# Optimization experiments

Hardware: AMD Instinct MI355X
Metric: run time of the kernel (lower is better)

## Reference

```python
import jax, jax.numpy as jnp
import numpy as np
from jax import lax

H = 256        # HIDDEN_DIM
H2 = 2 * H     # BiLSTM output dim
L = 100        # MAX_SENTENCE_LENGHT
B = 16
WE = 100       # word embed size
PE = 50        # pos embed size
VOC = 46       # POS_VOCAB_SIZE + 1
IN0 = WE + PE  # lstm layer-0 input dim


def setup_inputs():
    key = jax.random.key(0)
    ks = jax.random.split(key, 20)
    s = 0.05
    inp = {}
    inp["word_embeds"] = jax.random.normal(ks[0], (B, L, WE), jnp.float32)
    inp["pos_idx"] = jax.random.randint(ks[1], (B, L), 0, VOC)
    inp["sen_lens"] = jax.random.randint(ks[2], (B,), 1, L + 1)
    inp["pos_emb"] = jax.random.normal(ks[3], (VOC, PE), jnp.float32) * s
    # LSTM layer 0 (input dim 150), directions stacked on axis 0 (fwd, rev)
    inp["w_ih0"] = jax.random.normal(ks[4], (2, 4 * H, IN0), jnp.float32) * s
    inp["w_hh0"] = jax.random.normal(ks[5], (2, 4 * H, H), jnp.float32) * s
    inp["b_ih0"] = jax.random.normal(ks[6], (2, 4 * H), jnp.float32) * s
    inp["b_hh0"] = jax.random.normal(ks[7], (2, 4 * H), jnp.float32) * s
    # LSTM layers 1-3 (input dim 512): [layer, dir, ...]
    inp["w_ih"] = jax.random.normal(ks[8], (3, 2, 4 * H, H2), jnp.float32) * s
    inp["w_hh"] = jax.random.normal(ks[9], (3, 2, 4 * H, H), jnp.float32) * s
    inp["b_ih"] = jax.random.normal(ks[10], (3, 2, 4 * H), jnp.float32) * s
    inp["b_hh"] = jax.random.normal(ks[11], (3, 2, 4 * H), jnp.float32) * s
    # PosTagFC: Linear(1024,512), Linear(512,128), Linear(128,1)
    inp["W1"] = jax.random.normal(ks[12], (H2, 2 * H2), jnp.float32) * s
    inp["b1"] = jax.random.normal(ks[13], (H2,), jnp.float32) * s
    inp["W2"] = jax.random.normal(ks[14], (H // 2, H2), jnp.float32) * s
    inp["b2"] = jax.random.normal(ks[15], (H // 2,), jnp.float32) * s
    inp["W3"] = jax.random.normal(ks[16], (1, H // 2), jnp.float32) * s
    inp["b3"] = jax.random.normal(ks[17], (1,), jnp.float32) * s
    return inp


def _lstm_dir(x, wi, wh, bi, bh, reverse):
    # x: [B, L, F]; PyTorch gate order i, f, g, o
    gx = jnp.einsum('blf,gf->blg', x, wi) + bi + bh  # [B, L, 4H]
    xs = jnp.swapaxes(gx, 0, 1)                      # [L, B, 4H]
    if reverse:
        xs = xs[::-1]
    h0 = jnp.zeros((x.shape[0], H), x.dtype)
    def step(carry, g):
        h, c = carry
        g = g + h @ wh.T
        i, f, gg, o = jnp.split(g, 4, axis=-1)
        c = jax.nn.sigmoid(f) * c + jax.nn.sigmoid(i) * jnp.tanh(gg)
        h = jax.nn.sigmoid(o) * jnp.tanh(c)
        return (h, c), h
    _, hs = lax.scan(step, (h0, h0), xs)
    hs = jnp.swapaxes(hs, 0, 1)                      # [B, L, H]
    if reverse:
        hs = hs[:, ::-1]
    return hs


def _forward(word_embeds, pos_idx, sen_lens, pos_emb,
             w_ih0, w_hh0, b_ih0, b_hh0, w_ih, w_hh, b_ih, b_hh,
             W1, b1, W2, b2, W3, b3):
    x = jnp.concatenate([word_embeds, pos_emb[pos_idx]], axis=2)  # [B, L, 150]
    # 4-layer bidirectional LSTM (eval mode: inter-layer dropout off)
    fwd = _lstm_dir(x, w_ih0[0], w_hh0[0], b_ih0[0], b_hh0[0], False)
    bwd = _lstm_dir(x, w_ih0[1], w_hh0[1], b_ih0[1], b_hh0[1], True)
    x = jnp.concatenate([fwd, bwd], axis=-1)
    for l in range(3):
        fwd = _lstm_dir(x, w_ih[l, 0], w_hh[l, 0], b_ih[l, 0], b_hh[l, 0], False)
        bwd = _lstm_dir(x, w_ih[l, 1], w_hh[l, 1], b_ih[l, 1], b_hh[l, 1], True)
        x = jnp.concatenate([fwd, bwd], axis=-1)  # [B, L, 512]
    lstm_out = x
    # pairwise scoring: split W1 so we never materialize the 1024-dim concat
    rooted = jnp.concatenate([jnp.zeros((B, 1, H2), x.dtype), lstm_out], axis=1)  # [B, L+1, 512]
    W1a, W1b = W1[:, :H2], W1[:, H2:]
    h_first = lstm_out @ W1a.T          # [B, L, 512]
    h_root = rooted @ W1b.T             # [B, L+1, 512]
    h1 = jax.nn.relu(h_first[:, :, None, :] + h_root[:, None, :, :] + b1)  # [B, L, L+1, 512]
    h2 = jax.nn.relu(h1 @ W2.T + b2)    # [B, L, L+1, 128]
    sc = (h2 @ W3.T + b3)[..., 0]       # [B, L, L+1]
    # fill_diagonal_ on the [N,1] fc output zeroes only element 0 -> (0,0)
    sc = sc.at[:, 0, 0].set(0.0)
    row_ok = jnp.arange(L)[None, :] < sen_lens[:, None]        # [B, L]
    col_ok = jnp.arange(L + 1)[None, :] <= sen_lens[:, None]   # [B, L+1]
    sc = jnp.where(row_ok[:, :, None] & col_ok[:, None, :], sc, 0.0)
    return jnp.pad(sc, ((0, 0), (0, 1), (0, 0)))  # [B, 101, 101]


def reference(word_embeds, pos_idx, sen_lens, pos_emb,
              w_ih0, w_hh0, b_ih0, b_hh0, w_ih, w_hh, b_ih, b_hh,
              W1, b1, W2, b2, W3, b3):
    return _forward(word_embeds, pos_idx, sen_lens, pos_emb,
                    w_ih0, w_hh0, b_ih0, b_hh0, w_ih, w_hh, b_ih, b_hh,
                    W1, b1, W2, b2, W3, b3)
```

## Files before the change

kernel.cpp:

```cpp
#include <hip/hip_runtime.h>
#include <stdint.h>

#define NB 16
#define NL 100
#define NOUT (16*101*101)

typedef _Float16 f16x8 __attribute__((ext_vector_type(8)));
typedef float f32x4 __attribute__((ext_vector_type(4)));

__device__ __forceinline__ float sigm(float x) {
    x = fminf(fmaxf(x, -30.f), 30.f);
    return 1.f / (1.f + __expf(-x));
}
__device__ __forceinline__ float tanh_(float x) {
    x = fminf(fmaxf(x, -15.f), 15.f);
    float t = __expf(2.f * x);
    return (t - 1.f) / (t + 1.f);
}
__device__ __forceinline__ uint32_t pack2h(_Float16 a, _Float16 b) {
    return (uint32_t)__builtin_bit_cast(uint16_t, a) |
           ((uint32_t)__builtin_bit_cast(uint16_t, b) << 16);
}
#define MFMA16(A, B, C) __builtin_amdgcn_mfma_f32_16x16x32_f16( \
    __builtin_bit_cast(f16x8, A), (B), (C), 0, 0, 0)


__global__ __launch_bounds__(256) void pack_whh_mfma(const float* __restrict__ w_hh0,
                                                     const float* __restrict__ w_hh,
                                                     uint32_t* __restrict__ wpk) {
    int idx = blockIdx.x * 256 + threadIdx.x;
    if (idx >= 262144) return;
    int l6 = idx & 63;
    int kc = (idx >> 6) & 7;
    int mt = (idx >> 9) & 63;
    int ld = idx >> 15;
    int layer = ld >> 1, d = ld & 1;
    int row = mt * 16 + (l6 & 15);
    int k0 = kc * 32 + (l6 >> 4) * 8;
    const float* src = (layer == 0)
        ? &w_hh0[((size_t)d * 1024 + row) * 256]
        : &w_hh[(((size_t)(layer - 1) * 2 + d) * 1024 + row) * 256];
    uint4 o;
    o.x = pack2h((_Float16)src[k0 + 0], (_Float16)src[k0 + 1]);
    o.y = pack2h((_Float16)src[k0 + 2], (_Float16)src[k0 + 3]);
    o.z = pack2h((_Float16)src[k0 + 4], (_Float16)src[k0 + 5]);
    o.w = pack2h((_Float16)src[k0 + 6], (_Float16)src[k0 + 7]);
    *(uint4*)&wpk[(size_t)idx * 4] = o;
}

__global__ __launch_bounds__(256) void pack_wih(const float* __restrict__ w_ih0,
                                                const float* __restrict__ w_ih,
                                                uint32_t* __restrict__ wihpk) {
    int idx = blockIdx.x * 256 + threadIdx.x;
    if (idx >= 524288) return;
    int l6 = idx & 63;
    int kc = (idx >> 6) & 15;
    int mt = (idx >> 10) & 63;
    int dl = idx >> 16;
    int row = mt * 16 + (l6 & 15);
    int k0 = kc * 32 + (l6 >> 4) * 8;
    float v[8];
#pragma unroll
    for (int j = 0; j < 8; ++j) {
        int k = k0 + j;
        if (dl < 2) v[j] = (k < 150) ? w_ih0[((size_t)dl * 1024 + row) * 150 + k] : 0.f;
        else        v[j] = w_ih[((size_t)(dl - 2) * 1024 + row) * 512 + k];
    }
    uint4 o;
    o.x = pack2h((_Float16)v[0], (_Float16)v[1]);
    o.y = pack2h((_Float16)v[2], (_Float16)v[3]);
    o.z = pack2h((_Float16)v[4], (_Float16)v[5]);
    o.w = pack2h((_Float16)v[6], (_Float16)v[7]);
    *(uint4*)&wihpk[(size_t)idx * 4] = o;
}

__global__ __launch_bounds__(256) void pack_w1(const float* __restrict__ W1,
                                               uint32_t* __restrict__ w1pk) {
    int idx = blockIdx.x * 256 + threadIdx.x;
    if (idx >= 65536) return;
    int l6 = idx & 63;
    int kc = (idx >> 6) & 15;
    int mt = (idx >> 10) & 31;
    int half = idx >> 15;
    int row = mt * 16 + (l6 & 15);
    int k0 = kc * 32 + (l6 >> 4) * 8;
    const float* src = &W1[(size_t)row * 1024 + half * 512 + k0];
    uint4 o;
    o.x = pack2h((_Float16)src[0], (_Float16)src[1]);
    o.y = pack2h((_Float16)src[2], (_Float16)src[3]);
    o.z = pack2h((_Float16)src[4], (_Float16)src[5]);
    o.w = pack2h((_Float16)src[6], (_Float16)src[7]);
    *(uint4*)&w1pk[(size_t)idx * 4] = o;
}

__global__ __launch_bounds__(256) void pack_w2_mfma(const float* __restrict__ W2,
                                                    uint32_t* __restrict__ w2pk) {
    int idx = blockIdx.x * 256 + threadIdx.x;
    if (idx >= 16384) return;
    int l6 = idx & 63;
    int nt = (idx >> 6) & 7;
    int sp = (idx >> 9) & 1;
    int kc = idx >> 10;
    int ch = nt * 16 + (l6 & 15);
    int k0 = kc * 32 + (l6 >> 4) * 8;
    uint32_t dw[4];
#pragma unroll
    for (int dwi = 0; dwi < 4; ++dwi) {
        float x0 = W2[(size_t)ch * 512 + k0 + dwi * 2 + 0];
        float x1 = W2[(size_t)ch * 512 + k0 + dwi * 2 + 1];
        _Float16 h0 = (_Float16)x0, h1 = (_Float16)x1;
        _Float16 v0 = sp ? (_Float16)(x0 - (float)h0) : h0;
        _Float16 v1 = sp ? (_Float16)(x1 - (float)h1) : h1;
        dw[dwi] = pack2h(v0, v1);
    }
    *(uint4*)&w2pk[(size_t)idx * 4] = make_uint4(dw[0], dw[1], dw[2], dw[3]);
}

__global__ __launch_bounds__(256) void pack_bias(const float* __restrict__ b_ih0,
                                                 const float* __restrict__ b_hh0,
                                                 const float* __restrict__ b_ih,
                                                 const float* __restrict__ b_hh,
                                                 float* __restrict__ biasp) {
    int idx = blockIdx.x * 256 + threadIdx.x;
    if (idx >= 8 * 1024) return;
    int g = idx & 1023;
    int ld = idx >> 10;
    int l = ld >> 1, d = ld & 1;
    float v;
    if (l == 0) v = b_ih0[d * 1024 + g] + b_hh0[d * 1024 + g];
    else {
        size_t o = ((size_t)(l - 1) * 2 + d) * 1024 + g;
        v = b_ih[o] + b_hh[o];
    }
    biasp[idx] = v;
}

__global__ __launch_bounds__(256) void concat_x0v2(const float* __restrict__ we,
                                                   const int* __restrict__ pos_idx,
                                                   const float* __restrict__ pos_emb,
                                                   _Float16* __restrict__ xhi,
                                                   _Float16* __restrict__ xlo) {
    int idx = blockIdx.x * 256 + threadIdx.x;
    if (idx >= 1600 * 160) return;
    int mp = idx / 160, k = idx % 160;
    int tt = mp >> 4, b = mp & 15;
    float v;
    if (k < 100) v = we[((size_t)b * 100 + tt) * 100 + k];
    else if (k < 150) v = pos_emb[(size_t)pos_idx[b * 100 + tt] * 50 + (k - 100)];
    else v = 0.f;
    _Float16 hi = (_Float16)v;
    xhi[idx] = hi;
    xlo[idx] = (_Float16)(v - (float)hi);
}

__global__ __launch_bounds__(256) void zero_out(float* __restrict__ out) {
    int idx = blockIdx.x * 256 + threadIdx.x;
    if (idx < NOUT) out[idx] = 0.f;
}

__global__ __launch_bounds__(256) void gemm_gx(const _Float16* __restrict__ xhi,
                                               const _Float16* __restrict__ xlo,
                                               const uint32_t* __restrict__ wpk_base,
                                               const float* __restrict__ bias_base,
                                               float* __restrict__ gxf_base,
                                               int KC, int ldx) {
    const int d = blockIdx.z;
    const uint32_t* wpk = wpk_base + (size_t)d * 262144;
    const float* bias = bias_base + d * 1024;
    float* gxf_d = gxf_base + (size_t)d * 1638400;

    const int t = threadIdx.x;
    const int wv = t >> 6, l = t & 63;
    const int cgrp = l >> 4;
    const int m0t = blockIdx.x * 4;
    const int n0 = blockIdx.y * 64;
    const int tk0 = n0 + wv * 16 + (l & 15);

    f32x4 acc[4];
#pragma unroll
    for (int mt = 0; mt < 4; ++mt) acc[mt] = (f32x4){0.f, 0.f, 0.f, 0.f};

    for (int kc = 0; kc < KC; ++kc) {
        const int koff = kc * 32 + cgrp * 8;
        f16x8 bh = *(const f16x8*)&xhi[(size_t)tk0 * ldx + koff];
        f16x8 bl = *(const f16x8*)&xlo[(size_t)tk0 * ldx + koff];
#pragma unroll
        for (int mt = 0; mt < 4; ++mt) {
            uint4 a = *(const uint4*)&wpk[(((size_t)(m0t + mt) * 16 + kc) * 64 + l) * 4];
            acc[mt] = MFMA16(a, bh, acc[mt]);
            acc[mt] = MFMA16(a, bl, acc[mt]);
        }
    }
    const int b = l & 15;
    const int tt = tk0 >> 4;
#pragma unroll
    for (int mt = 0; mt < 4; ++mt) {
        int mtg = m0t + mt;
        f32x4 bv;
#pragma unroll
        for (int r = 0; r < 4; ++r) bv[r] = bias[mtg * 16 + cgrp * 4 + r];
        size_t off = ((size_t)b * 100 + tt) * 1024 + mtg * 16 + cgrp * 4;
        *(f32x4*)&gxf_d[off] = acc[mt] + bv;
    }
}

__global__ __launch_bounds__(256) void gemm_w1(const _Float16* __restrict__ xhi,
                                               const _Float16* __restrict__ xlo,
                                               const uint32_t* __restrict__ wpk_base,
                                               float* __restrict__ outp) {
    const int half = blockIdx.z;
    const uint32_t* wpk = wpk_base + (size_t)half * 131072;
    const int coff = half * 512;

    const int t = threadIdx.x;
    const int wv = t >> 6, l = t & 63;
    const int cgrp = l >> 4;
    const int m0t = blockIdx.x * 4;
    const int n0 = blockIdx.y * 64;
    const int tk0 = n0 + wv * 16 + (l & 15);

    f32x4 acc[4];
#pragma unroll
    for (int mt = 0; mt < 4; ++mt) acc[mt] = (f32x4){0.f, 0.f, 0.f, 0.f};

    for (int kc = 0; kc < 16; ++kc) {
        const int koff = kc * 32 + cgrp * 8;
        f16x8 bh = *(const f16x8*)&xhi[(size_t)tk0 * 512 + koff];
        f16x8 bl = *(const f16x8*)&xlo[(size_t)tk0 * 512 + koff];
#pragma unroll
        for (int mt = 0; mt < 4; ++mt) {
            uint4 a = *(const uint4*)&wpk[(((size_t)(m0t + mt) * 16 + kc) * 64 + l) * 4];
            acc[mt] = MFMA16(a, bh, acc[mt]);
            acc[mt] = MFMA16(a, bl, acc[mt]);
        }
    }
#pragma unroll
    for (int mt = 0; mt < 4; ++mt) {
        int mtg = m0t + mt;
        *(f32x4*)&outp[(size_t)tk0 * 1024 + coff + mtg * 16 + cgrp * 4] = acc[mt];
    }
}

__global__ __launch_bounds__(1024, 4) void lstm_v9(const float* __restrict__ gx,
                                                   const uint32_t* __restrict__ whhpk_layer,
                                                   _Float16* __restrict__ xhi,
                                                   _Float16* __restrict__ xlo) {
    extern __shared__ uint32_t smem[];
    uint32_t* wtail = smem;
    float*    gbuf  = (float*)(smem + 36864);
    uint32_t* hsta  = smem + 37888;

    const int d = blockIdx.x >> 4;
    const int b = blockIdx.x & 15;
    const int t = threadIdx.x;
    const int w = t >> 6;
    const int l = t & 63;
    const int cgrp = l >> 4;

    uint4 wreg[23];
    const uint32_t* wsrc = whhpk_layer + (size_t)d * 131072 + ((size_t)w * 4 * 8) * 256;
#pragma unroll
    for (int mtl = 0; mtl < 4; ++mtl)
#pragma unroll
        for (int kc = 0; kc < 8; ++kc) {
            int f = mtl * 8 + kc;
            uint4 v = *(const uint4*)&wsrc[((size_t)mtl * 8 + kc) * 256 + l * 4];
            if (f < 23) wreg[f] = v;
            else *(uint4*)&wtail[((w * 9 + (f - 23)) * 64 + l) * 4] = v;
        }
    if (t < 128) hsta[t] = 0u;
    float creg = 0.f;
    float gvi = 0.f, gvf = 0.f, gvg = 0.f, gvo = 0.f;
    const float* gxb = gx + ((size_t)(d * 16 + b)) * 102400;
    if (t < 256) {
        int tt0 = d ? NL - 1 : 0;
        gvi = gxb[(size_t)tt0 * 1024 + t];
        gvf = gxb[(size_t)tt0 * 1024 + 256 + t];
        gvg = gxb[(size_t)tt0 * 1024 + 512 + t];
        gvo = gxb[(size_t)tt0 * 1024 + 768 + t];
    }
    __syncthreads();

    for (int s = 0; s < NL; ++s) {
        const int tt = d ? (NL - 1 - s) : s;
        f32x4 acc0 = {0.f, 0.f, 0.f, 0.f};
        f32x4 acc1 = {0.f, 0.f, 0.f, 0.f};
        f32x4 acc2 = {0.f, 0.f, 0.f, 0.f};
        f32x4 acc3 = {0.f, 0.f, 0.f, 0.f};
#pragma unroll
        for (int kc = 0; kc < 8; ++kc) {
            uint4 braw = *(const uint4*)&hsta[kc * 16 + cgrp * 4];
            f16x8 B = __builtin_bit_cast(f16x8, braw);
            acc0 = MFMA16(wreg[kc], B, acc0);
            acc1 = MFMA16(wreg[8 + kc], B, acc1);
            uint4 a2raw = (kc < 7) ? wreg[16 + kc]
                                   : *(const uint4*)&wtail[((w * 9 + 0) * 64 + l) * 4];
            acc2 = MFMA16(a2raw, B, acc2);
            uint4 a3raw = *(const uint4*)&wtail[((w * 9 + kc + 1) * 64 + l) * 4];
            acc3 = MFMA16(a3raw, B, acc3);
        }
        if ((l & 15) == 0) {
            *(f32x4*)&gbuf[w * 64 +  0 + cgrp * 4] = acc0;
            *(f32x4*)&gbuf[w * 64 + 16 + cgrp * 4] = acc1;
            *(f32x4*)&gbuf[w * 64 + 32 + cgrp * 4] = acc2;
            *(f32x4*)&gbuf[w * 64 + 48 + cgrp * 4] = acc3;
        }
        __syncthreads();
        if (t < 256) {
            float gi = gbuf[t] + gvi;
            float gf = gbuf[256 + t] + gvf;
            float gg = gbuf[512 + t] + gvg;
            float go = gbuf[768 + t] + gvo;
            float cn = fmaf(sigm(gf), creg, sigm(gi) * tanh_(gg));
            creg = cn;
            float hn = sigm(go) * tanh_(cn);
            _Float16 hh = (_Float16)hn;
            ((_Float16*)hsta)[t] = hh;
            const size_t xb = ((size_t)tt * 16 + b) * 512 + d * 256 + t;
            xhi[xb] = hh;
            xlo[xb] = (_Float16)(hn - (float)hh);
            if (s + 1 < NL) {
                int tn = d ? (NL - 2 - s) : (s + 1);
                gvi = gxb[(size_t)tn * 1024 + t];
                gvf = gxb[(size_t)tn * 1024 + 256 + t];
                gvg = gxb[(size_t)tn * 1024 + 512 + t];
                gvo = gxb[(size_t)tn * 1024 + 768 + t];
            }
        }
        __syncthreads();
    }
}

__global__ __launch_bounds__(256) void scorer_v2(const float* __restrict__ hfr,
                                                 const uint32_t* __restrict__ w2pk,
                                                 const float* __restrict__ b1,
                                                 const float* __restrict__ b2,
                                                 const float* __restrict__ W3,
                                                 const float* __restrict__ b3,
                                                 const int* __restrict__ sen_lens,
                                                 float* __restrict__ out) {
    __shared__ float hfs[16][520];
    __shared__ float hrs[8][520];

    const int t = threadIdx.x;
    const int wv = t >> 6, l = t & 63;
    const int cgrp = l >> 4;
    const int b = blockIdx.z;
    const int i0 = blockIdx.x * 16;
    const int j0 = blockIdx.y * 8;

#pragma unroll
    for (int rep = 0; rep < 8; ++rep) {
        int slot = rep * 256 + t;
        int row = slot >> 7, c4 = slot & 127;
        int i = i0 + row;
        float4 v = make_float4(0.f, 0.f, 0.f, 0.f);
        if (i < 100) v = *(const float4*)&hfr[((size_t)(i * 16 + b)) * 1024 + c4 * 4];
        *(float4*)&hfs[row][c4 * 4] = v;
    }
#pragma unroll
    for (int rep = 0; rep < 4; ++rep) {
        int slot = rep * 256 + t;
        int row = slot >> 7, c4 = slot & 127;
        int j = j0 + row;
        float4 bv = *(const float4*)&b1[c4 * 4];
        float4 v = make_float4(0.f, 0.f, 0.f, 0.f);
        if (j >= 1 && j <= 100)
            v = *(const float4*)&hfr[((size_t)((j - 1) * 16 + b)) * 1024 + 512 + c4 * 4];
        v.x += bv.x; v.y += bv.y; v.z += bv.z; v.w += bv.w;
        *(float4*)&hrs[row][c4 * 4] = v;
    }

    float b2r[8], w3r[8];
#pragma unroll
    for (int nt = 0; nt < 8; ++nt) {
        b2r[nt] = b2[nt * 16 + (l & 15)];
        w3r[nt] = W3[nt * 16 + (l & 15)];
    }
    f32x4 accA[8], accB[8];
#pragma unroll
    for (int nt = 0; nt < 8; ++nt) {
        accA[nt] = (f32x4){0.f, 0.f, 0.f, 0.f};
        accB[nt] = (f32x4){0.f, 0.f, 0.f, 0.f};
    }
    const int p0 = (wv * 2) * 16 + (l & 15);
    const int p1 = (wv * 2 + 1) * 16 + (l & 15);
    const int ilA = p0 >> 3, jlA = p0 & 7;
    const int ilB = p1 >> 3, jlB = p1 & 7;
    __syncthreads();

    for (int kc = 0; kc < 16; ++kc) {
        const int k0 = kc * 32 + cgrp * 8;
        f16x8 ahi0, alo0, ahi1, alo1;
        {
            f32x4 f0 = *(const f32x4*)&hfs[ilA][k0];
            f32x4 f1 = *(const f32x4*)&hfs[ilA][k0 + 4];
            f32x4 r0 = *(const f32x4*)&hrs[jlA][k0];
            f32x4 r1 = *(const f32x4*)&hrs[jlA][k0 + 4];
#pragma unroll
            for (int j = 0; j < 4; ++j) {
                float v = fmaxf(f0[j] + r0[j], 0.f);
                _Float16 hi = (_Float16)v;
                ahi0[j] = hi; alo0[j] = (_Float16)(v - (float)hi);
                v = fmaxf(f1[j] + r1[j], 0.f);
                hi = (_Float16)v;
                ahi0[4 + j] = hi; alo0[4 + j] = (_Float16)(v - (float)hi);
            }
        }
        {
            f32x4 f0 = *(const f32x4*)&hfs[ilB][k0];
            f32x4 f1 = *(const f32x4*)&hfs[ilB][k0 + 4];
            f32x4 r0 = *(const f32x4*)&hrs[jlB][k0];
            f32x4 r1 = *(const f32x4*)&hrs[jlB][k0 + 4];
#pragma unroll
            for (int j = 0; j < 4; ++j) {
                float v = fmaxf(f0[j] + r0[j], 0.f);
                _Float16 hi = (_Float16)v;
                ahi1[j] = hi; alo1[j] = (_Float16)(v - (float)hi);
                v = fmaxf(f1[j] + r1[j], 0.f);
                hi = (_Float16)v;
                ahi1[4 + j] = hi; alo1[4 + j] = (_Float16)(v - (float)hi);
            }
        }
#pragma unroll
        for (int nt = 0; nt < 8; ++nt) {
            f16x8 bhi = __builtin_bit_cast(f16x8,
                *(const uint4*)&w2pk[((((size_t)kc * 2 + 0) * 8 + nt) * 64 + l) * 4]);
            f16x8 blo = __builtin_bit_cast(f16x8,
                *(const uint4*)&w2pk[((((size_t)kc * 2 + 1) * 8 + nt) * 64 + l) * 4]);
            accA[nt] = __builtin_amdgcn_mfma_f32_16x16x32_f16(ahi0, bhi, accA[nt], 0, 0, 0);
            accA[nt] = __builtin_amdgcn_mfma_f32_16x16x32_f16(ahi0, blo, accA[nt], 0, 0, 0);
            accA[nt] = __builtin_amdgcn_mfma_f32_16x16x32_f16(alo0, bhi, accA[nt], 0, 0, 0);
            accB[nt] = __builtin_amdgcn_mfma_f32_16x16x32_f16(ahi1, bhi, accB[nt], 0, 0, 0);
            accB[nt] = __builtin_amdgcn_mfma_f32_16x16x32_f16(ahi1, blo, accB[nt], 0, 0, 0);
            accB[nt] = __builtin_amdgcn_mfma_f32_16x16x32_f16(alo1, bhi, accB[nt], 0, 0, 0);
        }
    }
    float sp0[4] = {0.f, 0.f, 0.f, 0.f};
    float sp1[4] = {0.f, 0.f, 0.f, 0.f};
#pragma unroll
    for (int nt = 0; nt < 8; ++nt)
#pragma unroll
        for (int r = 0; r < 4; ++r) {
            sp0[r] += fmaxf(accA[nt][r] + b2r[nt], 0.f) * w3r[nt];
            sp1[r] += fmaxf(accB[nt][r] + b2r[nt], 0.f) * w3r[nt];
        }
#pragma unroll
    for (int r = 0; r < 4; ++r) {
#pragma unroll
        for (int off = 1; off < 16; off <<= 1) {
            sp0[r] += __shfl_xor(sp0[r], off);
            sp1[r] += __shfl_xor(sp1[r], off);
        }
    }
    if ((l & 15) == 0) {
        float bias3 = b3[0];
        int sl = sen_lens[b];
#pragma unroll
        for (int mtl = 0; mtl < 2; ++mtl)
#pragma unroll
            for (int r = 0; r < 4; ++r) {
                int p = (wv * 2 + mtl) * 16 + cgrp * 4 + r;
                int i = i0 + (p >> 3), j = j0 + (p & 7);
                if (i < 100 && j < 101) {
                    float v = (mtl == 0 ? sp0[r] : sp1[r]) + bias3;
                    if (!((i < sl) && (j <= sl)) || (i == 0 && j == 0)) v = 0.f;
                    out[((size_t)b * 101 + i) * 101 + j] = v;
                }
            }
    }
}

extern "C" void kernel_launch(void* const* d_in, const int* in_sizes, int n_in,
                              void* d_out, int out_size, void* d_ws, size_t ws_size,
                              hipStream_t stream) {
    const float* we       = (const float*)d_in[0];
    const int*   pos_idx  = (const int*)d_in[1];
    const int*   sen_lens = (const int*)d_in[2];
    const float* pos_emb  = (const float*)d_in[3];
    const float* w_ih0    = (const float*)d_in[4];
    const float* w_hh0    = (const float*)d_in[5];
    const float* b_ih0    = (const float*)d_in[6];
    const float* b_hh0    = (const float*)d_in[7];
    const float* w_ih     = (const float*)d_in[8];
    const float* w_hh     = (const float*)d_in[9];
    const float* b_ih     = (const float*)d_in[10];
    const float* b_hh     = (const float*)d_in[11];
    const float* W1       = (const float*)d_in[12];
    const float* b1       = (const float*)d_in[13];
    const float* W2       = (const float*)d_in[14];
    const float* b2       = (const float*)d_in[15];
    const float* W3       = (const float*)d_in[16];
    const float* b3       = (const float*)d_in[17];
    float* out = (float*)d_out;

    uint32_t* ws = (uint32_t*)d_ws;
    _Float16* x0hi  = (_Float16*)(ws + 0);
    _Float16* x0lo  = (_Float16*)(ws + 128000);
    float*    gxf   = (float*)(ws + 256000);
    _Float16* xAhi  = (_Float16*)(ws + 3532800);
    _Float16* xAlo  = (_Float16*)(ws + 3942400);
    _Float16* xBhi  = (_Float16*)(ws + 5171200);
    _Float16* xBlo  = (_Float16*)(ws + 5580800);
    float*    hfr   = (float*)(ws + 6809600);
    uint32_t* wihpk = ws + 8448000;
    uint32_t* whhpk = ws + 10545152;
    uint32_t* w2pk  = ws + 11593728;
    float*    biasp = (float*)(ws + 11659264);

    pack_whh_mfma<<<1024, 256, 0, stream>>>(w_hh0, w_hh, whhpk);
    pack_wih<<<2048, 256, 0, stream>>>(w_ih0, w_ih, wihpk);
    pack_w2_mfma<<<64, 256, 0, stream>>>(W2, w2pk);
    pack_bias<<<32, 256, 0, stream>>>(b_ih0, b_hh0, b_ih, b_hh, biasp);
    concat_x0v2<<<1000, 256, 0, stream>>>(we, pos_idx, pos_emb, x0hi, x0lo);

    const int LSTM_SMEM = 38016 * 4;

    gemm_gx<<<dim3(16, 25, 2), 256, 0, stream>>>(
        x0hi, x0lo, wihpk, biasp, gxf, 5, 160);
    lstm_v9<<<32, 1024, LSTM_SMEM, stream>>>(gxf, whhpk, xAhi, xAlo);

    _Float16* xih = xAhi; _Float16* xil = xAlo;
    _Float16* xoh = xBhi; _Float16* xol = xBlo;
    for (int lyr = 1; lyr < 4; ++lyr) {
        int dlbase = 2 + (lyr - 1) * 2;
        gemm_gx<<<dim3(16, 25, 2), 256, 0, stream>>>(
            xih, xil, wihpk + (size_t)dlbase * 262144,
            biasp + lyr * 2048, gxf, 16, 512);
        lstm_v9<<<32, 1024, LSTM_SMEM, stream>>>(gxf, whhpk + (size_t)lyr * 262144,
                                                 xoh, xol);
        _Float16* th = xih; xih = xoh; xoh = th;
        _Float16* tl = xil; xil = xol; xol = tl;
    }

    uint32_t* w1pk = (uint32_t*)gxf;
    pack_w1<<<256, 256, 0, stream>>>(W1, w1pk);
    gemm_w1<<<dim3(8, 25, 2), 256, 0, stream>>>(xih, xil, w1pk, hfr);

    zero_out<<<(NOUT + 255) / 256, 256, 0, stream>>>(out);
    scorer_v2<<<dim3(7, 13, 16), 256, 0, stream>>>(hfr, w2pk, b1, b2, W3, b3,
                                                   sen_lens, out);
}
```

Measured before the change: 999.1 us.

## Merge pack kernels, shrink output zeroing, move LSTM hidden state to global

Five separate weight/bias/input packing kernels become one launch, cutting launch overhead. The full output zeroing becomes a kernel that zeroes only the padded last row, which assumes the scorer writes every other element. The LSTM recurrent hidden state moves from shared memory to a per-block global buffer. That move risks a visibility problem, since global writes may not be seen by other threads after __syncthreads without a fence or cache bypass, and it adds latency on the recurrence critical path.

```diff
diff --git a/kernel.cpp b/kernel.cpp
--- a/kernel.cpp
+++ b/kernel.cpp
@@ -24,54 +24,107 @@
 #define MFMA16(A, B, C) __builtin_amdgcn_mfma_f32_16x16x32_f16( \
     __builtin_bit_cast(f16x8, A), (B), (C), 0, 0, 0)
 
-
-__global__ __launch_bounds__(256) void pack_whh_mfma(const float* __restrict__ w_hh0,
-                                                     const float* __restrict__ w_hh,
-                                                     uint32_t* __restrict__ wpk) {
-    int idx = blockIdx.x * 256 + threadIdx.x;
-    if (idx >= 262144) return;
-    int l6 = idx & 63;
-    int kc = (idx >> 6) & 7;
-    int mt = (idx >> 9) & 63;
-    int ld = idx >> 15;
-    int layer = ld >> 1, d = ld & 1;
-    int row = mt * 16 + (l6 & 15);
-    int k0 = kc * 32 + (l6 >> 4) * 8;
-    const float* src = (layer == 0)
-        ? &w_hh0[((size_t)d * 1024 + row) * 256]
-        : &w_hh[(((size_t)(layer - 1) * 2 + d) * 1024 + row) * 256];
-    uint4 o;
-    o.x = pack2h((_Float16)src[k0 + 0], (_Float16)src[k0 + 1]);
-    o.y = pack2h((_Float16)src[k0 + 2], (_Float16)src[k0 + 3]);
-    o.z = pack2h((_Float16)src[k0 + 4], (_Float16)src[k0 + 5]);
-    o.w = pack2h((_Float16)src[k0 + 6], (_Float16)src[k0 + 7]);
-    *(uint4*)&wpk[(size_t)idx * 4] = o;
-}
-
-__global__ __launch_bounds__(256) void pack_wih(const float* __restrict__ w_ih0,
+__global__ __launch_bounds__(256) void pack_all(const float* __restrict__ w_hh0,
+                                                const float* __restrict__ w_hh,
+                                                const float* __restrict__ w_ih0,
                                                 const float* __restrict__ w_ih,
-                                                uint32_t* __restrict__ wihpk) {
-    int idx = blockIdx.x * 256 + threadIdx.x;
-    if (idx >= 524288) return;
-    int l6 = idx & 63;
-    int kc = (idx >> 6) & 15;
-    int mt = (idx >> 10) & 63;
-    int dl = idx >> 16;
-    int row = mt * 16 + (l6 & 15);
-    int k0 = kc * 32 + (l6 >> 4) * 8;
-    float v[8];
-#pragma unroll
-    for (int j = 0; j < 8; ++j) {
-        int k = k0 + j;
-        if (dl < 2) v[j] = (k < 150) ? w_ih0[((size_t)dl * 1024 + row) * 150 + k] : 0.f;
-        else        v[j] = w_ih[((size_t)(dl - 2) * 1024 + row) * 512 + k];
-    }
-    uint4 o;
-    o.x = pack2h((_Float16)v[0], (_Float16)v[1]);
-    o.y = pack2h((_Float16)v[2], (_Float16)v[3]);
-    o.z = pack2h((_Float16)v[4], (_Float16)v[5]);
-    o.w = pack2h((_Float16)v[6], (_Float16)v[7]);
-    *(uint4*)&wihpk[(size_t)idx * 4] = o;
+                                                const float* __restrict__ W2,
+                                                const float* __restrict__ b_ih0,
+                                                const float* __restrict__ b_hh0,
+                                                const float* __restrict__ b_ih,
+                                                const float* __restrict__ b_hh,
+                                                const float* __restrict__ we,
+                                                const int* __restrict__ pos_idx,
+                                                const float* __restrict__ pos_emb,
+                                                uint32_t* __restrict__ whhpk,
+                                                uint32_t* __restrict__ wihpk,
+                                                uint32_t* __restrict__ w2pk,
+                                                float* __restrict__ biasp,
+                                                _Float16* __restrict__ xhi,
+                                                _Float16* __restrict__ xlo) {
+    int gid = blockIdx.x * 256 + threadIdx.x;
+    if (gid < 262144) {
+        int idx = gid;
+        int l6 = idx & 63;
+        int kc = (idx >> 6) & 7;
+        int mt = (idx >> 9) & 63;
+        int ld = idx >> 15;
+        int layer = ld >> 1, d = ld & 1;
+        int row = mt * 16 + (l6 & 15);
+        int k0 = kc * 32 + (l6 >> 4) * 8;
+        const float* src = (layer == 0)
+            ? &w_hh0[((size_t)d * 1024 + row) * 256]
+            : &w_hh[(((size_t)(layer - 1) * 2 + d) * 1024 + row) * 256];
+        uint4 o;
+        o.x = pack2h((_Float16)src[k0 + 0], (_Float16)src[k0 + 1]);
+        o.y = pack2h((_Float16)src[k0 + 2], (_Float16)src[k0 + 3]);
+        o.z = pack2h((_Float16)src[k0 + 4], (_Float16)src[k0 + 5]);
+        o.w = pack2h((_Float16)src[k0 + 6], (_Float16)src[k0 + 7]);
+        *(uint4*)&whhpk[(size_t)idx * 4] = o;
+    } else if (gid < 786432) {
+        int idx = gid - 262144;
+        int l6 = idx & 63;
+        int kc = (idx >> 6) & 15;
+        int mt = (idx >> 10) & 63;
+        int dl = idx >> 16;
+        int row = mt * 16 + (l6 & 15);
+        int k0 = kc * 32 + (l6 >> 4) * 8;
+        float v[8];
+#pragma unroll
+        for (int j = 0; j < 8; ++j) {
+            int k = k0 + j;
+            if (dl < 2) v[j] = (k < 150) ? w_ih0[((size_t)dl * 1024 + row) * 150 + k] : 0.f;
+            else        v[j] = w_ih[((size_t)(dl - 2) * 1024 + row) * 512 + k];
+        }
+        uint4 o;
+        o.x = pack2h((_Float16)v[0], (_Float16)v[1]);
+        o.y = pack2h((_Float16)v[2], (_Float16)v[3]);
+        o.z = pack2h((_Float16)v[4], (_Float16)v[5]);
+        o.w = pack2h((_Float16)v[6], (_Float16)v[7]);
+        *(uint4*)&wihpk[(size_t)idx * 4] = o;
+    } else if (gid < 802816) {
+        int idx = gid - 786432;
+        int l6 = idx & 63;
+        int nt = (idx >> 6) & 7;
+        int sp = (idx >> 9) & 1;
+        int kc = idx >> 10;
+        int ch = nt * 16 + (l6 & 15);
+        int k0 = kc * 32 + (l6 >> 4) * 8;
+        uint32_t dw[4];
+#pragma unroll
+        for (int dwi = 0; dwi < 4; ++dwi) {
+            float x0 = W2[(size_t)ch * 512 + k0 + dwi * 2 + 0];
+            float x1 = W2[(size_t)ch * 512 + k0 + dwi * 2 + 1];
+            _Float16 h0 = (_Float16)x0, h1 = (_Float16)x1;
+            _Float16 v0 = sp ? (_Float16)(x0 - (float)h0) : h0;
+            _Float16 v1 = sp ? (_Float16)(x1 - (float)h1) : h1;
+            dw[dwi] = pack2h(v0, v1);
+        }
+        *(uint4*)&w2pk[(size_t)idx * 4] = make_uint4(dw[0], dw[1], dw[2], dw[3]);
+    } else if (gid < 811008) {
+        int idx = gid - 802816;
+        int g = idx & 1023;
+        int ld = idx >> 10;
+        int l = ld >> 1, d = ld & 1;
+        float v;
+        if (l == 0) v = b_ih0[d * 1024 + g] + b_hh0[d * 1024 + g];
+        else {
+            size_t o = ((size_t)(l - 1) * 2 + d) * 1024 + g;
+            v = b_ih[o] + b_hh[o];
+        }
+        biasp[idx] = v;
+    } else if (gid < 1067008) {
+        int idx = gid - 811008;
+        int mp = idx / 160, k = idx % 160;
+        int tt = mp >> 4, b = mp & 15;
+        float v;
+        if (k < 100) v = we[((size_t)b * 100 + tt) * 100 + k];
+        else if (k < 150) v = pos_emb[(size_t)pos_idx[b * 100 + tt] * 50 + (k - 100)];
+        else v = 0.f;
+        _Float16 hi = (_Float16)v;
+        xhi[idx] = hi;
+        xlo[idx] = (_Float16)(v - (float)hi);
+    }
 }
 
 __global__ __launch_bounds__(256) void pack_w1(const float* __restrict__ W1,
@@ -93,69 +146,12 @@
     *(uint4*)&w1pk[(size_t)idx * 4] = o;
 }
 
-__global__ __launch_bounds__(256) void pack_w2_mfma(const float* __restrict__ W2,
-                                                    uint32_t* __restrict__ w2pk) {
+__global__ __launch_bounds__(256) void zero_pad(float* __restrict__ out) {
     int idx = blockIdx.x * 256 + threadIdx.x;
-    if (idx >= 16384) return;
-    int l6 = idx & 63;
-    int nt = (idx >> 6) & 7;
-    int sp = (idx >> 9) & 1;
-    int kc = idx >> 10;
-    int ch = nt * 16 + (l6 & 15);
-    int k0 = kc * 32 + (l6 >> 4) * 8;
-    uint32_t dw[4];
-#pragma unroll
-    for (int dwi = 0; dwi < 4; ++dwi) {
-        float x0 = W2[(size_t)ch * 512 + k0 + dwi * 2 + 0];
-        float x1 = W2[(size_t)ch * 512 + k0 + dwi * 2 + 1];
-        _Float16 h0 = (_Float16)x0, h1 = (_Float16)x1;
-        _Float16 v0 = sp ? (_Float16)(x0 - (float)h0) : h0;
-        _Float16 v1 = sp ? (_Float16)(x1 - (float)h1) : h1;
-        dw[dwi] = pack2h(v0, v1);
-    }
-    *(uint4*)&w2pk[(size_t)idx * 4] = make_uint4(dw[0], dw[1], dw[2], dw[3]);
-}
-
-__global__ __launch_bounds__(256) void pack_bias(const float* __restrict__ b_ih0,
-                                                 const float* __restrict__ b_hh0,
-                                                 const float* __restrict__ b_ih,
-                                                 const float* __restrict__ b_hh,
-                                                 float* __restrict__ biasp) {
-    int idx = blockIdx.x * 256 + threadIdx.x;
-    if (idx >= 8 * 1024) return;
-    int g = idx & 1023;
-    int ld = idx >> 10;
-    int l = ld >> 1, d = ld & 1;
-    float v;
-    if (l == 0) v = b_ih0[d * 1024 + g] + b_hh0[d * 1024 + g];
-    else {
-        size_t o = ((size_t)(l - 1) * 2 + d) * 1024 + g;
-        v = b_ih[o] + b_hh[o];
-    }
-    biasp[idx] = v;
-}
-
-__global__ __launch_bounds__(256) void concat_x0v2(const float* __restrict__ we,
-                                                   const int* __restrict__ pos_idx,
-                                                   const float* __restrict__ pos_emb,
-                                                   _Float16* __restrict__ xhi,
-                                                   _Float16* __restrict__ xlo) {
-    int idx = blockIdx.x * 256 + threadIdx.x;
-    if (idx >= 1600 * 160) return;
-    int mp = idx / 160, k = idx % 160;
-    int tt = mp >> 4, b = mp & 15;
-    float v;
-    if (k < 100) v = we[((size_t)b * 100 + tt) * 100 + k];
-    else if (k < 150) v = pos_emb[(size_t)pos_idx[b * 100 + tt] * 50 + (k - 100)];
-    else v = 0.f;
-    _Float16 hi = (_Float16)v;
-    xhi[idx] = hi;
-    xlo[idx] = (_Float16)(v - (float)hi);
-}
-
-__global__ __launch_bounds__(256) void zero_out(float* __restrict__ out) {
-    int idx = blockIdx.x * 256 + threadIdx.x;
-    if (idx < NOUT) out[idx] = 0.f;
+    if (idx < 16 * 101) {
+        int b = idx / 101, j = idx % 101;
+        out[((size_t)b * 101 + 100) * 101 + j] = 0.f;
+    }
 }
 
 __global__ __launch_bounds__(256) void gemm_gx(const _Float16* __restrict__ xhi,
@@ -241,14 +237,14 @@
     }
 }
 
-__global__ __launch_bounds__(1024, 4) void lstm_v9(const float* __restrict__ gx,
-                                                   const uint32_t* __restrict__ whhpk_layer,
-                                                   _Float16* __restrict__ xhi,
-                                                   _Float16* __restrict__ xlo) {
+__global__ __launch_bounds__(1024, 4) void lstm_v11(const float* __restrict__ gx,
+                                                    const uint32_t* __restrict__ whhpk_layer,
+                                                    _Float16* __restrict__ hgl,
+                                                    _Float16* __restrict__ xhi,
+                                                    _Float16* __restrict__ xlo) {
     extern __shared__ uint32_t smem[];
     uint32_t* wtail = smem;
     float*    gbuf  = (float*)(smem + 36864);
-    uint32_t* hsta  = smem + 37888;
 
     const int d = blockIdx.x >> 4;
     const int b = blockIdx.x & 15;
@@ -268,7 +264,9 @@
             if (f < 23) wreg[f] = v;
             else *(uint4*)&wtail[((w * 9 + (f - 23)) * 64 + l) * 4] = v;
         }
-    if (t < 128) hsta[t] = 0u;
+    _Float16* hg = hgl + (size_t)(d * 16 + b) * 256;
+    const uint4* hg4 = (const uint4*)hg;
+    if (t < 128) ((uint32_t*)hg)[t] = 0u;
     float creg = 0.f;
     float gvi = 0.f, gvf = 0.f, gvg = 0.f, gvo = 0.f;
     const float* gxb = gx + ((size_t)(d * 16 + b)) * 102400;
@@ -289,7 +287,7 @@
         f32x4 acc3 = {0.f, 0.f, 0.f, 0.f};
 #pragma unroll
         for (int kc = 0; kc < 8; ++kc) {
-            uint4 braw = *(const uint4*)&hsta[kc * 16 + cgrp * 4];
+            uint4 braw = hg4[kc * 4 + cgrp];
             f16x8 B = __builtin_bit_cast(f16x8, braw);
             acc0 = MFMA16(wreg[kc], B, acc0);
             acc1 = MFMA16(wreg[8 + kc], B, acc1);
@@ -315,7 +313,7 @@
             creg = cn;
             float hn = sigm(go) * tanh_(cn);
             _Float16 hh = (_Float16)hn;
-            ((_Float16*)hsta)[t] = hh;
+            hg[t] = hh;
             const size_t xb = ((size_t)tt * 16 + b) * 512 + d * 256 + t;
             xhi[xb] = hh;
             xlo[xb] = (_Float16)(hn - (float)hh);
@@ -507,18 +505,18 @@
     uint32_t* whhpk = ws + 10545152;
     uint32_t* w2pk  = ws + 11593728;
     float*    biasp = (float*)(ws + 11659264);
-
-    pack_whh_mfma<<<1024, 256, 0, stream>>>(w_hh0, w_hh, whhpk);
-    pack_wih<<<2048, 256, 0, stream>>>(w_ih0, w_ih, wihpk);
-    pack_w2_mfma<<<64, 256, 0, stream>>>(W2, w2pk);
-    pack_bias<<<32, 256, 0, stream>>>(b_ih0, b_hh0, b_ih, b_hh, biasp);
-    concat_x0v2<<<1000, 256, 0, stream>>>(we, pos_idx, pos_emb, x0hi, x0lo);
-
-    const int LSTM_SMEM = 38016 * 4;
+    _Float16* hgl   = (_Float16*)(ws + 11667456);
+
+    pack_all<<<4168, 256, 0, stream>>>(w_hh0, w_hh, w_ih0, w_ih, W2,
+                                       b_ih0, b_hh0, b_ih, b_hh,
+                                       we, pos_idx, pos_emb,
+                                       whhpk, wihpk, w2pk, biasp, x0hi, x0lo);
+
+    const int LSTM_SMEM = 37888 * 4;
 
     gemm_gx<<<dim3(16, 25, 2), 256, 0, stream>>>(
         x0hi, x0lo, wihpk, biasp, gxf, 5, 160);
-    lstm_v9<<<32, 1024, LSTM_SMEM, stream>>>(gxf, whhpk, xAhi, xAlo);
+    lstm_v11<<<32, 1024, LSTM_SMEM, stream>>>(gxf, whhpk, hgl, xAhi, xAlo);
 
     _Float16* xih = xAhi; _Float16* xil = xAlo;
     _Float16* xoh = xBhi; _Float16* xol = xBlo;
@@ -527,8 +525,8 @@
         gemm_gx<<<dim3(16, 25, 2), 256, 0, stream>>>(
             xih, xil, wihpk + (size_t)dlbase * 262144,
             biasp + lyr * 2048, gxf, 16, 512);
-        lstm_v9<<<32, 1024, LSTM_SMEM, stream>>>(gxf, whhpk + (size_t)lyr * 262144,
-                                                 xoh, xol);
+        lstm_v11<<<32, 1024, LSTM_SMEM, stream>>>(gxf, whhpk + (size_t)lyr * 262144,
+                                                  hgl, xoh, xol);
         _Float16* th = xih; xih = xoh; xoh = th;
         _Float16* tl = xil; xil = xol; xol = tl;
     }
@@ -537,7 +535,7 @@
     pack_w1<<<256, 256, 0, stream>>>(W1, w1pk);
     gemm_w1<<<dim3(8, 25, 2), 256, 0, stream>>>(xih, xil, w1pk, hfr);
 
-    zero_out<<<(NOUT + 255) / 256, 256, 0, stream>>>(out);
+    zero_pad<<<7, 256, 0, stream>>>(out);
     scorer_v2<<<dim3(7, 13, 16), 256, 0, stream>>>(hfr, w2pk, b1, b2, W3, b3,
                                                    sen_lens, out);
 }
```

Measured after the change: 1.256 ms. 1.26x slower.
